# Performance work log

Measured on AMD Instinct MI355X. Metric: run time of the kernel, lower is better.

The kernel has to match this reference:

```python
import jax, jax.numpy as jnp
import numpy as np

B, L, E, H, A = 32, 4096, 512, 512, 256


def setup_inputs() -> dict:
    key = jax.random.key(0)
    ks = jax.random.split(key, 8)
    s_e = 1.0 / np.sqrt(E)
    s_h = 1.0 / np.sqrt(H)
    s_a = 1.0 / np.sqrt(A)
    return {
        "features": jax.random.normal(ks[0], (B, L, E), jnp.float32),
        "decoder_hidden": jax.random.normal(ks[1], (B, H), jnp.float32),
        "W_enc": jax.random.uniform(ks[2], (E, A), jnp.float32, -s_e, s_e),
        "b_enc": jax.random.uniform(ks[3], (A,), jnp.float32, -s_e, s_e),
        "W_dec": jax.random.uniform(ks[4], (H, A), jnp.float32, -s_h, s_h),
        "b_dec": jax.random.uniform(ks[5], (A,), jnp.float32, -s_h, s_h),
        "W_v": jax.random.uniform(ks[6], (A, 1), jnp.float32, -s_a, s_a),
        "b_v": jax.random.uniform(ks[7], (1,), jnp.float32, -s_a, s_a),
    }


def reference(features, decoder_hidden, W_enc, b_enc, W_dec, b_dec, W_v, b_v):
    # encoder/decoder projections
    enc_attn = jnp.einsum("ble,ea->bla", features, W_enc) + b_enc  # [B,L,A]
    dec_attn = decoder_hidden @ W_dec + b_dec                       # [B,A]
    sim = jax.nn.relu(enc_attn + dec_attn[:, None, :])              # [B,L,A]
    scores = (jnp.einsum("bla,ao->blo", sim, W_v) + b_v)[..., 0]    # [B,L]
    attn_weights = jax.nn.softmax(scores, axis=1)                   # [B,L]
    output = jnp.einsum("ble,bl->be", features, attn_weights)       # [B,E]
    return output, attn_weights
```

## Files before the change

kernel.cpp:

```cpp
#include <hip/hip_runtime.h>
#include <hip/hip_bf16.h>
#include <stdint.h>


typedef __attribute__((ext_vector_type(8))) short bf16x8;
typedef __attribute__((ext_vector_type(4))) float f32x4;

__device__ __forceinline__ unsigned short f32_to_bf16(float f) {
    union { float f; unsigned u; } v; v.f = f;
    unsigned u = v.u;
    u += 0x7fffu + ((u >> 16) & 1u);
    return (unsigned short)(u >> 16);
}

__device__ __forceinline__ void async_load16(const void* g, void* l) {
    __builtin_amdgcn_global_load_lds(
        (const __attribute__((address_space(1))) unsigned int*)g,
        (__attribute__((address_space(3))) unsigned int*)l, 16, 0, 0);
}

__global__ __launch_bounds__(256) void prep_kernel(
    const float* __restrict__ dh, const float* __restrict__ W_enc,
    const float* __restrict__ b_enc, const float* __restrict__ W_dec,
    const float* __restrict__ b_dec, unsigned short* __restrict__ Wp,
    float* __restrict__ dec_full)
{
    int t = threadIdx.x;
    if (blockIdx.x < 32) {
        int b = blockIdx.x;
        float a0 = 0.f, a1 = 0.f, a2 = 0.f, a3 = 0.f;
        #pragma unroll 2
        for (int h = 0; h < 512; h += 4) {
            a0 += dh[b * 512 + h + 0] * W_dec[(h + 0) * 256 + t];
            a1 += dh[b * 512 + h + 1] * W_dec[(h + 1) * 256 + t];
            a2 += dh[b * 512 + h + 2] * W_dec[(h + 2) * 256 + t];
            a3 += dh[b * 512 + h + 3] * W_dec[(h + 3) * 256 + t];
        }
        dec_full[b * 256 + t] = (a0 + a1) + (a2 + a3) + b_enc[t] + b_dec[t];
    } else {
        int tid = (blockIdx.x - 32) * 256 + t;
        #pragma unroll
        for (int i = 0; i < 8; ++i) {
            int d = tid + i * 16384;
            int j = d & 7;
            int n = (d >> 3) & 255;
            int chunk = (d >> 11) & 7;
            int kb = d >> 14;
            int k = kb * 64 + chunk * 8 + j;
            Wp[d] = f32_to_bf16(W_enc[k * 256 + n]);
        }
    }
}

__global__ __launch_bounds__(256, 2) void score_kernel(
    const float* __restrict__ feat, const unsigned short* __restrict__ Wp,
    const float* __restrict__ dec_full, const float* __restrict__ W_v,
    float* __restrict__ scores, float* __restrict__ m_c,
    float* __restrict__ o_part)
{
    __shared__ unsigned short Alds[8192];
    __shared__ unsigned short Blds[16384];
    __shared__ float red[4][128];
    __shared__ float sblk[128];
    __shared__ float wexp[128];
    __shared__ float mshr;
    __shared__ float red2x[128], red2y[128], red2z[128], red2w[128];

    const int t = threadIdx.x;
    const int lane = t & 63;
    const int wave = t >> 6;
    const int r0 = blockIdx.x * 128;
    const int b = r0 >> 12;

    float wv[4], dec[4];
    #pragma unroll
    for (int ct = 0; ct < 4; ++ct) {
        int a = wave * 64 + ct * 16 + (lane & 15);
        wv[ct] = W_v[a];
        dec[ct] = dec_full[b * 256 + a];
    }

    f32x4 acc[8][4];
    #pragma unroll
    for (int mt = 0; mt < 8; ++mt)
        #pragma unroll
        for (int ct = 0; ct < 4; ++ct)
            acc[mt][ct] = f32x4{0.f, 0.f, 0.f, 0.f};

    float4 av[8];
    #pragma unroll
    for (int it = 0; it < 8; ++it) {
        int lin = it * 256 + t;
        int m = lin >> 4, kq = lin & 15;
        av[it] = *(const float4*)(feat + (size_t)(r0 + m) * 512 + kq * 4);
    }

    for (int ks = 0; ks < 8; ++ks) {
        #pragma unroll
        for (int q = 0; q < 8; ++q) {
            int c = q * 256 + wave * 64 + lane;
            async_load16(Wp + ks * 16384 + c * 8, Blds + c * 8);
        }
        #pragma unroll
        for (int it = 0; it < 8; ++it) {
            int lin = it * 256 + t;
            int m = lin >> 4, kq = lin & 15;
            ushort4 w;
            w.x = f32_to_bf16(av[it].x);
            w.y = f32_to_bf16(av[it].y);
            w.z = f32_to_bf16(av[it].z);
            w.w = f32_to_bf16(av[it].w);
            int chunk = kq >> 1, jh = kq & 1;
            *(ushort4*)(Alds + m * 64 + ((chunk ^ (m & 7)) * 8) + jh * 4) = w;
        }
        __syncthreads();
        if (ks < 7) {
            #pragma unroll
            for (int it = 0; it < 8; ++it) {
                int lin = it * 256 + t;
                int m = lin >> 4, kq = lin & 15;
                av[it] = *(const float4*)(feat + (size_t)(r0 + m) * 512 + (ks + 1) * 64 + kq * 4);
            }
        }
        #pragma unroll
        for (int kk = 0; kk < 2; ++kk) {
            int chunk = kk * 4 + (lane >> 4);
            bf16x8 bfr[4];
            #pragma unroll
            for (int ct = 0; ct < 4; ++ct) {
                int n = wave * 64 + ct * 16 + (lane & 15);
                bfr[ct] = *(const bf16x8*)(Blds + (chunk * 256 + n) * 8);
            }
            #pragma unroll
            for (int mt = 0; mt < 8; ++mt) {
                int m = mt * 16 + (lane & 15);
                bf16x8 afr = *(const bf16x8*)(Alds + m * 64 + ((chunk ^ (m & 7)) * 8));
                #pragma unroll
                for (int ct = 0; ct < 4; ++ct)
                    acc[mt][ct] = __builtin_amdgcn_mfma_f32_16x16x32_bf16(
                        afr, bfr[ct], acc[mt][ct], 0, 0, 0);
            }
        }
        __syncthreads();
    }

    #pragma unroll
    for (int mt = 0; mt < 8; ++mt) {
        #pragma unroll
        for (int r = 0; r < 4; ++r) {
            float p = 0.f;
            #pragma unroll
            for (int ct = 0; ct < 4; ++ct) {
                float v = acc[mt][ct][r] + dec[ct];
                v = v > 0.f ? v : 0.f;
                p += v * wv[ct];
            }
            p += __shfl_xor(p, 1);
            p += __shfl_xor(p, 2);
            p += __shfl_xor(p, 4);
            p += __shfl_xor(p, 8);
            if ((lane & 15) == 0)
                red[wave][mt * 16 + (lane >> 4) * 4 + r] = p;
        }
    }
    __syncthreads();
    if (t < 128) {
        float v = red[0][t] + red[1][t] + red[2][t] + red[3][t];
        sblk[t] = v;
        scores[r0 + t] = v;
    }
    __syncthreads();
    if (t < 64) {
        float m = fmaxf(sblk[t], sblk[t + 64]);
        #pragma unroll
        for (int o = 1; o < 64; o <<= 1) m = fmaxf(m, __shfl_xor(m, o));
        if (t == 0) mshr = m;
    }
    __syncthreads();
    float mb = mshr;
    if (t < 128) wexp[t] = __expf(sblk[t] - mb);
    __syncthreads();

    int e4 = t & 127, lh = t >> 7;
    float ax = 0.f, ay = 0.f, az = 0.f, aw = 0.f;
    #pragma unroll 8
    for (int i = 0; i < 64; ++i) {
        int l = i * 2 + lh;
        float wl = wexp[l];
        const float4 f = *(const float4*)(feat + (size_t)(r0 + l) * 512 + e4 * 4);
        ax += wl * f.x; ay += wl * f.y; az += wl * f.z; aw += wl * f.w;
    }
    if (lh) { red2x[e4] = ax; red2y[e4] = ay; red2z[e4] = az; red2w[e4] = aw; }
    __syncthreads();
    if (!lh) {
        float4 r;
        r.x = ax + red2x[e4]; r.y = ay + red2y[e4];
        r.z = az + red2z[e4]; r.w = aw + red2w[e4];
        *(float4*)(o_part + (size_t)blockIdx.x * 512 + e4 * 4) = r;
        if (t == 0) m_c[blockIdx.x] = mb;
    }
}

__global__ __launch_bounds__(256) void softmax_kernel(
    const float* __restrict__ scores, float* __restrict__ out,
    float* __restrict__ MZ)
{
    __shared__ float sred[4];
    __shared__ float zred[4];
    int b = blockIdx.x, t = threadIdx.x;

    const float* s = scores + b * 4096;
    float vals[16];
    float m = -1e30f;
    #pragma unroll
    for (int i = 0; i < 16; ++i) { vals[i] = s[t + i * 256]; m = fmaxf(m, vals[i]); }
    #pragma unroll
    for (int o = 1; o < 64; o <<= 1) m = fmaxf(m, __shfl_xor(m, o));
    if ((t & 63) == 0) sred[t >> 6] = m;
    __syncthreads();
    m = fmaxf(fmaxf(sred[0], sred[1]), fmaxf(sred[2], sred[3]));

    float z = 0.f;
    #pragma unroll
    for (int i = 0; i < 16; ++i) { vals[i] = __expf(vals[i] - m); z += vals[i]; }
    #pragma unroll
    for (int o = 1; o < 64; o <<= 1) z += __shfl_xor(z, o);
    if ((t & 63) == 0) zred[t >> 6] = z;
    __syncthreads();
    z = zred[0] + zred[1] + zred[2] + zred[3];
    float inv = 1.f / z;
    #pragma unroll
    for (int i = 0; i < 16; ++i)
        out[16384 + b * 4096 + t + i * 256] = vals[i] * inv;
    if (t == 0) { MZ[b] = m; MZ[32 + b] = z; }
}

__global__ __launch_bounds__(256) void combine_kernel(
    const float* __restrict__ o_part, const float* __restrict__ m_c,
    const float* __restrict__ MZ, float* __restrict__ out)
{
    __shared__ float sc[32];
    int b = blockIdx.x, t = threadIdx.x;
    if (t < 32) sc[t] = __expf(m_c[b * 32 + t] - MZ[b]) * (1.f / MZ[32 + b]);
    __syncthreads();
    float a0 = 0.f, a1 = 0.f;
    #pragma unroll 8
    for (int c = 0; c < 32; ++c) {
        const float2 v = *(const float2*)(o_part + (size_t)(b * 32 + c) * 512 + t * 2);
        a0 += sc[c] * v.x; a1 += sc[c] * v.y;
    }
    float2 r; r.x = a0; r.y = a1;
    *(float2*)(out + b * 512 + t * 2) = r;
}

extern "C" void kernel_launch(void* const* d_in, const int* in_sizes, int n_in,
                              void* d_out, int out_size, void* d_ws, size_t ws_size,
                              hipStream_t stream) {
    const float* feat  = (const float*)d_in[0];
    const float* dh    = (const float*)d_in[1];
    const float* W_enc = (const float*)d_in[2];
    const float* b_enc = (const float*)d_in[3];
    const float* W_dec = (const float*)d_in[4];
    const float* b_dec = (const float*)d_in[5];
    const float* W_v   = (const float*)d_in[6];

    unsigned short* Wp = (unsigned short*)d_ws;
    float* dec_full = (float*)((char*)d_ws + 262144);
    float* scores   = (float*)((char*)d_ws + 294912);
    float* m_c      = (float*)((char*)d_ws + 819200);
    float* MZ       = (float*)((char*)d_ws + 823296);
    float* o_part   = (float*)((char*)d_ws + 1048576);
    float* out      = (float*)d_out;

    prep_kernel<<<96, 256, 0, stream>>>(dh, W_enc, b_enc, W_dec, b_dec, Wp, dec_full);
    score_kernel<<<1024, 256, 0, stream>>>(feat, Wp, dec_full, W_v, scores, m_c, o_part);
    softmax_kernel<<<32, 256, 0, stream>>>(scores, out, MZ);
    combine_kernel<<<32, 256, 0, stream>>>(o_part, m_c, MZ, out);
}
```

Measured before the change: 444.7 us.

## Fuse softmax and combine into score kernel via last-block atomic counter

Removes the separate softmax and combine launches. Each score block increments a per-batch atomic counter, and the last block to finish for a batch does the softmax normalisation and the weighted combine of partial outputs. The prep kernel resets the counters and now stages decoder_hidden in shared memory with 8 accumulators. This saves two launches and their gaps, at the cost of a tail where a single block per batch does serial work and relies on acquire/release ordering for correctness.

```diff
diff --git a/kernel.cpp b/kernel.cpp
--- a/kernel.cpp
+++ b/kernel.cpp
@@ -23,20 +23,31 @@
     const float* __restrict__ dh, const float* __restrict__ W_enc,
     const float* __restrict__ b_enc, const float* __restrict__ W_dec,
     const float* __restrict__ b_dec, unsigned short* __restrict__ Wp,
-    float* __restrict__ dec_full)
+    float* __restrict__ dec_full, unsigned* __restrict__ cnt)
 {
     int t = threadIdx.x;
     if (blockIdx.x < 32) {
         int b = blockIdx.x;
+        if (b == 0 && t < 32) cnt[t] = 0;
+        __shared__ float dhs[512];
+        dhs[t]       = dh[b * 512 + t];
+        dhs[t + 256] = dh[b * 512 + 256 + t];
+        __syncthreads();
         float a0 = 0.f, a1 = 0.f, a2 = 0.f, a3 = 0.f;
-        #pragma unroll 2
-        for (int h = 0; h < 512; h += 4) {
-            a0 += dh[b * 512 + h + 0] * W_dec[(h + 0) * 256 + t];
-            a1 += dh[b * 512 + h + 1] * W_dec[(h + 1) * 256 + t];
-            a2 += dh[b * 512 + h + 2] * W_dec[(h + 2) * 256 + t];
-            a3 += dh[b * 512 + h + 3] * W_dec[(h + 3) * 256 + t];
-        }
-        dec_full[b * 256 + t] = (a0 + a1) + (a2 + a3) + b_enc[t] + b_dec[t];
+        float a4 = 0.f, a5 = 0.f, a6 = 0.f, a7 = 0.f;
+        #pragma unroll 4
+        for (int h = 0; h < 512; h += 8) {
+            a0 += dhs[h + 0] * W_dec[(h + 0) * 256 + t];
+            a1 += dhs[h + 1] * W_dec[(h + 1) * 256 + t];
+            a2 += dhs[h + 2] * W_dec[(h + 2) * 256 + t];
+            a3 += dhs[h + 3] * W_dec[(h + 3) * 256 + t];
+            a4 += dhs[h + 4] * W_dec[(h + 4) * 256 + t];
+            a5 += dhs[h + 5] * W_dec[(h + 5) * 256 + t];
+            a6 += dhs[h + 6] * W_dec[(h + 6) * 256 + t];
+            a7 += dhs[h + 7] * W_dec[(h + 7) * 256 + t];
+        }
+        dec_full[b * 256 + t] =
+            ((a0 + a1) + (a2 + a3)) + ((a4 + a5) + (a6 + a7)) + b_enc[t] + b_dec[t];
     } else {
         int tid = (blockIdx.x - 32) * 256 + t;
         #pragma unroll
@@ -56,7 +67,8 @@
     const float* __restrict__ feat, const unsigned short* __restrict__ Wp,
     const float* __restrict__ dec_full, const float* __restrict__ W_v,
     float* __restrict__ scores, float* __restrict__ m_c,
-    float* __restrict__ o_part)
+    float* __restrict__ o_part, unsigned* __restrict__ cnt,
+    float* __restrict__ out)
 {
     __shared__ unsigned short Alds[8192];
     __shared__ unsigned short Blds[16384];
@@ -65,6 +77,7 @@
     __shared__ float wexp[128];
     __shared__ float mshr;
     __shared__ float red2x[128], red2y[128], red2z[128], red2w[128];
+    __shared__ unsigned dflag;
 
     const int t = threadIdx.x;
     const int lane = t & 63;
@@ -199,15 +212,16 @@
         *(float4*)(o_part + (size_t)blockIdx.x * 512 + e4 * 4) = r;
         if (t == 0) m_c[blockIdx.x] = mb;
     }
-}
-
-__global__ __launch_bounds__(256) void softmax_kernel(
-    const float* __restrict__ scores, float* __restrict__ out,
-    float* __restrict__ MZ)
-{
-    __shared__ float sred[4];
-    __shared__ float zred[4];
-    int b = blockIdx.x, t = threadIdx.x;
+
+    __syncthreads();
+    if (t == 0) {
+        unsigned old = __hip_atomic_fetch_add(cnt + b, 1u,
+                                              __ATOMIC_ACQ_REL,
+                                              __HIP_MEMORY_SCOPE_AGENT);
+        dflag = (old == 31u) ? 1u : 0u;
+    }
+    __syncthreads();
+    if (!dflag) return;
 
     const float* s = scores + b * 4096;
     float vals[16];
@@ -216,41 +230,33 @@
     for (int i = 0; i < 16; ++i) { vals[i] = s[t + i * 256]; m = fmaxf(m, vals[i]); }
     #pragma unroll
     for (int o = 1; o < 64; o <<= 1) m = fmaxf(m, __shfl_xor(m, o));
-    if ((t & 63) == 0) sred[t >> 6] = m;
-    __syncthreads();
-    m = fmaxf(fmaxf(sred[0], sred[1]), fmaxf(sred[2], sred[3]));
+    if ((t & 63) == 0) red[0][t >> 6] = m;
+    __syncthreads();
+    m = fmaxf(fmaxf(red[0][0], red[0][1]), fmaxf(red[0][2], red[0][3]));
 
     float z = 0.f;
     #pragma unroll
     for (int i = 0; i < 16; ++i) { vals[i] = __expf(vals[i] - m); z += vals[i]; }
     #pragma unroll
     for (int o = 1; o < 64; o <<= 1) z += __shfl_xor(z, o);
-    if ((t & 63) == 0) zred[t >> 6] = z;
-    __syncthreads();
-    z = zred[0] + zred[1] + zred[2] + zred[3];
-    float inv = 1.f / z;
+    if ((t & 63) == 0) red[1][t >> 6] = z;
+    __syncthreads();
+    z = red[1][0] + red[1][1] + red[1][2] + red[1][3];
+    float invz = 1.f / z;
     #pragma unroll
     for (int i = 0; i < 16; ++i)
-        out[16384 + b * 4096 + t + i * 256] = vals[i] * inv;
-    if (t == 0) { MZ[b] = m; MZ[32 + b] = z; }
-}
-
-__global__ __launch_bounds__(256) void combine_kernel(
-    const float* __restrict__ o_part, const float* __restrict__ m_c,
-    const float* __restrict__ MZ, float* __restrict__ out)
-{
-    __shared__ float sc[32];
-    int b = blockIdx.x, t = threadIdx.x;
-    if (t < 32) sc[t] = __expf(m_c[b * 32 + t] - MZ[b]) * (1.f / MZ[32 + b]);
+        out[16384 + b * 4096 + t + i * 256] = vals[i] * invz;
+
+    if (t < 32) red[2][t] = __expf(m_c[b * 32 + t] - m) * invz;
     __syncthreads();
     float a0 = 0.f, a1 = 0.f;
     #pragma unroll 8
     for (int c = 0; c < 32; ++c) {
         const float2 v = *(const float2*)(o_part + (size_t)(b * 32 + c) * 512 + t * 2);
-        a0 += sc[c] * v.x; a1 += sc[c] * v.y;
-    }
-    float2 r; r.x = a0; r.y = a1;
-    *(float2*)(out + b * 512 + t * 2) = r;
+        a0 += red[2][c] * v.x; a1 += red[2][c] * v.y;
+    }
+    float2 r2; r2.x = a0; r2.y = a1;
+    *(float2*)(out + b * 512 + t * 2) = r2;
 }
 
 extern "C" void kernel_launch(void* const* d_in, const int* in_sizes, int n_in,
@@ -268,12 +274,11 @@
     float* dec_full = (float*)((char*)d_ws + 262144);
     float* scores   = (float*)((char*)d_ws + 294912);
     float* m_c      = (float*)((char*)d_ws + 819200);
-    float* MZ       = (float*)((char*)d_ws + 823296);
+    unsigned* cnt   = (unsigned*)((char*)d_ws + 823296);
     float* o_part   = (float*)((char*)d_ws + 1048576);
     float* out      = (float*)d_out;
 
-    prep_kernel<<<96, 256, 0, stream>>>(dh, W_enc, b_enc, W_dec, b_dec, Wp, dec_full);
-    score_kernel<<<1024, 256, 0, stream>>>(feat, Wp, dec_full, W_v, scores, m_c, o_part);
-    softmax_kernel<<<32, 256, 0, stream>>>(scores, out, MZ);
-    combine_kernel<<<32, 256, 0, stream>>>(o_part, m_c, MZ, out);
-}
+    prep_kernel<<<96, 256, 0, stream>>>(dh, W_enc, b_enc, W_dec, b_dec, Wp, dec_full, cnt);
+    score_kernel<<<1024, 256, 0, stream>>>(feat, Wp, dec_full, W_v, scores, m_c,
+                                           o_part, cnt, out);
+}
```

New measurement: 461.2 us. +3.7%, slower.
